# Kernel optimization log

Measured on AMD Instinct MI355X. Metric: run time of the kernel, lower is better.

## Reference

```python
import jax, jax.numpy as jnp
import numpy as np

N = 100000      # nodes
E = 1600000     # edges (avg degree 16)
IN = 128        # in_channels
H = 128         # hidden_channels
EPS = 1e-5      # BatchNorm eps


def setup_inputs() -> dict:
    key = jax.random.key(0)
    ks = jax.random.split(key, 10)
    x = jax.random.normal(ks[0], (N, IN), jnp.float32)
    edge_index = jax.random.randint(ks[1], (2, E), 0, N, dtype=jnp.int32)

    def lin(k, i, o):
        return jax.random.normal(k, (i, o), jnp.float32) * (1.0 / np.sqrt(i))

    d2 = 2 * H
    return {
        "x": x, "edge_index": edge_index,
        # SAGEConv 1: 128 -> 128
        "w1l": lin(ks[2], IN, H), "w1r": lin(ks[3], IN, H), "b1": jnp.zeros((H,), jnp.float32),
        "g1": jnp.ones((H,), jnp.float32), "be1": jnp.zeros((H,), jnp.float32),
        "m1": jnp.zeros((H,), jnp.float32), "v1": jnp.ones((H,), jnp.float32),
        # SAGEConv 2: 128 -> 256
        "w2l": lin(ks[4], H, d2), "w2r": lin(ks[5], H, d2), "b2": jnp.zeros((d2,), jnp.float32),
        "g2": jnp.ones((d2,), jnp.float32), "be2": jnp.zeros((d2,), jnp.float32),
        "m2": jnp.zeros((d2,), jnp.float32), "v2": jnp.ones((d2,), jnp.float32),
        # SAGEConv 3: 256 -> 256
        "w3l": lin(ks[6], d2, d2), "w3r": lin(ks[7], d2, d2), "b3": jnp.zeros((d2,), jnp.float32),
        "g3": jnp.ones((d2,), jnp.float32), "be3": jnp.zeros((d2,), jnp.float32),
        "m3": jnp.zeros((d2,), jnp.float32), "v3": jnp.ones((d2,), jnp.float32),
    }


def _sage_conv(x, src, dst, wl, wr, b):
    # PyG SAGEConv (mean aggr): out = mean_{j in N(i)} x_j @ W_l + x_i @ W_r + b
    agg = jax.ops.segment_sum(x[src], dst, num_segments=N)          # [N, d_in]
    deg = jax.ops.segment_sum(jnp.ones((src.shape[0],), x.dtype), dst, num_segments=N)
    mean = agg / jnp.maximum(deg, 1.0)[:, None]
    return mean @ wl + x @ wr + b


def _bn(x, g, b, m, v):
    # BatchNorm1d in eval mode (running stats); dropout is a no-op in eval
    return (x - m) * jax.lax.rsqrt(v + EPS) * g + b


def reference(x, edge_index,
              w1l, w1r, b1, g1, be1, m1, v1,
              w2l, w2r, b2, g2, be2, m2, v2,
              w3l, w3r, b3, g3, be3, m3, v3):
    src, dst = edge_index[0], edge_index[1]
    h = _bn(jax.nn.relu(_sage_conv(x, src, dst, w1l, w1r, b1)), g1, be1, m1, v1)
    h = _bn(jax.nn.relu(_sage_conv(h, src, dst, w2l, w2r, b2)), g2, be2, m2, v2)
    h = _bn(jax.nn.relu(_sage_conv(h, src, dst, w3l, w3r, b3)), g3, be3, m3, v3)
    return h  # [N, 2*H]
```

## Files before the change

kernel.cpp:

```cpp
#include <hip/hip_runtime.h>

#define NNODES 100000
#define NEDGES 1600000
#define EPSV 1e-5f

#define NB   391
#define BCAP 4608
#define EPB  4096

typedef __attribute__((ext_vector_type(8))) short bf16x8;
typedef __attribute__((ext_vector_type(4))) float f32x4;

__device__ __forceinline__ float bf2f(uint hi_shifted) {
    union { uint u; float f; } c; c.u = hi_shifted; return c.f;
}
__device__ __forceinline__ ushort f2bf(float f) {
    union { float f; uint u; } c; c.f = f;
    uint u = c.u;
    return (ushort)((u + 0x7fffu + ((u >> 16) & 1u)) >> 16);
}
__device__ __forceinline__ uint pack2(float f0, float f1) {
    return (uint)f2bf(f0) | ((uint)f2bf(f1) << 16);
}
__device__ __forceinline__ void acc8(float* a, uint4 v) {
    a[0] += bf2f(v.x << 16); a[1] += bf2f(v.x & 0xffff0000u);
    a[2] += bf2f(v.y << 16); a[3] += bf2f(v.y & 0xffff0000u);
    a[4] += bf2f(v.z << 16); a[5] += bf2f(v.z & 0xffff0000u);
    a[6] += bf2f(v.w << 16); a[7] += bf2f(v.w & 0xffff0000u);
}

__global__ __launch_bounds__(256) void part_kernel(
    const int* __restrict__ src, const int* __restrict__ dst,
    int* __restrict__ cursor, uint2* __restrict__ pairs, int E)
{
    __shared__ int lcnt[NB];
    __shared__ int lbase[NB];
    const int t = threadIdx.x;
    for (int i = t; i < NB; i += 256) lcnt[i] = 0;
    __syncthreads();

    const int base = blockIdx.x * EPB;
    const int lim  = min(base + EPB, E);

    for (int e = base + t; e < lim; e += 256)
        atomicAdd(&lcnt[((unsigned)dst[e]) >> 8], 1);
    __syncthreads();

    for (int i = t; i < NB; i += 256) {
        int c = lcnt[i];
        lbase[i] = c ? atomicAdd(&cursor[i], c) : 0;
        lcnt[i] = 0;
    }
    __syncthreads();

    for (int e = base + t; e < lim; e += 256) {
        int d = dst[e];
        int b = ((unsigned)d) >> 8;
        int p = lbase[b] + atomicAdd(&lcnt[b], 1);
        if (p < BCAP) pairs[(size_t)b * BCAP + p] = make_uint2((uint)src[e], (uint)d);
    }
}

__global__ __launch_bounds__(512) void bscan_kernel(const int* __restrict__ cursor,
                                                    int* __restrict__ colBase)
{
    __shared__ int s[512];
    int t = threadIdx.x;
    int v = (t < NB) ? min(cursor[t], BCAP) : 0;
    s[t] = v;
    __syncthreads();
    #pragma unroll
    for (int off = 1; off < 512; off <<= 1) {
        int a = (t >= off) ? s[t - off] : 0;
        __syncthreads();
        s[t] += a;
        __syncthreads();
    }
    if (t < NB) colBase[t] = s[t] - v;
}

__global__ __launch_bounds__(256) void csr_fin_kernel(
    const uint2* __restrict__ pairs, const int* __restrict__ cursor,
    const int* __restrict__ colBase, int* __restrict__ cnt,
    int* __restrict__ rptr, int* __restrict__ col, int n)
{
    __shared__ int lcnt[256];
    __shared__ int lofs[256];
    const int b = blockIdx.x;
    const int t = threadIdx.x;
    const int ecnt  = min(cursor[b], BCAP);
    const int cbase = colBase[b];
    const uint2* __restrict__ pp = pairs + (size_t)b * BCAP;

    lcnt[t] = 0;
    __syncthreads();
    for (int e = t; e < ecnt; e += 256)
        atomicAdd(&lcnt[pp[e].y & 255u], 1);
    __syncthreads();

    const int v = lcnt[t];
    lofs[t] = v;
    __syncthreads();
    #pragma unroll
    for (int off = 1; off < 256; off <<= 1) {
        int a = (t >= off) ? lofs[t - off] : 0;
        __syncthreads();
        lofs[t] += a;
        __syncthreads();
    }
    const int excl = lofs[t] - v;

    const int node = (b << 8) + t;
    if (node < n) {
        cnt[node]  = v;
        rptr[node] = cbase + excl + v;
    }
    __syncthreads();
    lcnt[t] = excl;
    __syncthreads();

    for (int e = t; e < ecnt; e += 256) {
        uint2 pr = pp[e];
        int p = cbase + atomicAdd(&lcnt[pr.y & 255u], 1);
        col[p] = (int)pr.x;
    }
}

__global__ void cvt_bf_kernel(const float* __restrict__ in, ushort* __restrict__ out, int n4) {
    int i = blockIdx.x * blockDim.x + threadIdx.x;
    if (i < n4) {
        float4 v = ((const float4*)in)[i];
        ushort4 o;
        o.x = f2bf(v.x); o.y = f2bf(v.y); o.z = f2bf(v.z); o.w = f2bf(v.w);
        ((ushort4*)out)[i] = o;
    }
}

__global__ void wT_all_kernel(
    const float* __restrict__ w1l, const float* __restrict__ w1r,
    const float* __restrict__ w2l, const float* __restrict__ w2r,
    const float* __restrict__ w3l, const float* __restrict__ w3r,
    ushort* __restrict__ t1l, ushort* __restrict__ t1r,
    ushort* __restrict__ t2l, ushort* __restrict__ t2r,
    ushort* __restrict__ t3l, ushort* __restrict__ t3r)
{
    int idx = blockIdx.x * blockDim.x + threadIdx.x;
    const float* w; ushort* wt; int K, Nout, i;
    if      (idx <  16384) { w = w1l; wt = t1l; K = 128; Nout = 128; i = idx; }
    else if (idx <  32768) { w = w1r; wt = t1r; K = 128; Nout = 128; i = idx - 16384; }
    else if (idx <  65536) { w = w2l; wt = t2l; K = 128; Nout = 256; i = idx - 32768; }
    else if (idx <  98304) { w = w2r; wt = t2r; K = 128; Nout = 256; i = idx - 65536; }
    else if (idx < 163840) { w = w3l; wt = t3l; K = 256; Nout = 256; i = idx - 98304; }
    else if (idx < 229376) { w = w3r; wt = t3r; K = 256; Nout = 256; i = idx - 163840; }
    else return;
    int k = i / Nout, n = i - k * Nout;
    wt[(size_t)n * K + k] = f2bf(w[i]);
}

template<int D>
__global__ __launch_bounds__(256) void gather_bf(
    const ushort* __restrict__ x, const int* __restrict__ rptr,
    const int* __restrict__ cnt, const int* __restrict__ col,
    ushort* __restrict__ agg, int n)
{
    constexpr int TPN = D / 8;
    constexpr int NPB = 256 / TPN;
    const int node = blockIdx.x * NPB + threadIdx.x / TPN;
    const int lane = threadIdx.x % TPN;
    if (node >= n) return;

    const int c   = cnt[node];
    const int end = rptr[node];
    const uint4* __restrict__ xp = (const uint4*)x + lane;

    float a[8] = {};
    int e = end - c;
    for (; e + 3 < end; e += 4) {
        int s0 = col[e], s1 = col[e + 1], s2 = col[e + 2], s3 = col[e + 3];
        uint4 v0 = xp[(size_t)s0 * TPN];
        uint4 v1 = xp[(size_t)s1 * TPN];
        uint4 v2 = xp[(size_t)s2 * TPN];
        uint4 v3 = xp[(size_t)s3 * TPN];
        acc8(a, v0); acc8(a, v1); acc8(a, v2); acc8(a, v3);
    }
    for (; e < end; ++e) acc8(a, xp[(size_t)col[e] * TPN]);

    const float inv = 1.0f / fmaxf((float)c, 1.0f);
    uint4 o;
    o.x = pack2(a[0] * inv, a[1] * inv);
    o.y = pack2(a[2] * inv, a[3] * inv);
    o.z = pack2(a[4] * inv, a[5] * inv);
    o.w = pack2(a[6] * inv, a[7] * inv);
    ((uint4*)agg)[(size_t)node * TPN + lane] = o;
}

template<int DIN, int DOUT, bool OUTF32>
__global__ __launch_bounds__(256) void mfma_layer(
    const ushort* __restrict__ xin, const ushort* __restrict__ agg,
    const ushort* __restrict__ wlT, const ushort* __restrict__ wrT,
    const float* __restrict__ bias, const float* __restrict__ gamma,
    const float* __restrict__ beta, const float* __restrict__ rmean,
    const float* __restrict__ rvar, void* __restrict__ outp, int M)
{
    constexpr int BM = 128, BN = 128, BK = 32;
    constexpr int LDA = BK + 8;
    __shared__ ushort As[BM * LDA];
    __shared__ ushort Bs[BN * LDA];

    const int tid  = threadIdx.x;
    const int lane = tid & 63;
    const int wid  = tid >> 6;
    const int wm   = (wid & 1) * 64;
    const int wn   = (wid >> 1) * 64;
    const int lr   = lane & 15;
    const int quad = lane >> 4;

    const int row0 = blockIdx.x * BM;
    const int col0 = blockIdx.y * BN;

    f32x4 acc[4][4] = {};

    const int s_row  = tid >> 2;
    const int s_koff = (tid & 3) * 8;

    #pragma unroll
    for (int phase = 0; phase < 2; ++phase) {
        const ushort* __restrict__ A = phase ? xin : agg;
        const ushort* __restrict__ W = phase ? wrT : wlT;

        for (int k0 = 0; k0 < DIN; k0 += BK) {
            int gr0 = row0 + s_row;       gr0 = gr0 < M ? gr0 : M - 1;
            int gr1 = row0 + s_row + 64;  gr1 = gr1 < M ? gr1 : M - 1;
            uint4 a0v = *(const uint4*)(A + (size_t)gr0 * DIN + k0 + s_koff);
            uint4 a1v = *(const uint4*)(A + (size_t)gr1 * DIN + k0 + s_koff);
            uint4 b0v = *(const uint4*)(W + (size_t)(col0 + s_row) * DIN + k0 + s_koff);
            uint4 b1v = *(const uint4*)(W + (size_t)(col0 + s_row + 64) * DIN + k0 + s_koff);

            __syncthreads();
            *(uint4*)&As[s_row * LDA + s_koff]        = a0v;
            *(uint4*)&As[(s_row + 64) * LDA + s_koff] = a1v;
            *(uint4*)&Bs[s_row * LDA + s_koff]        = b0v;
            *(uint4*)&Bs[(s_row + 64) * LDA + s_koff] = b1v;
            __syncthreads();

            bf16x8 af[4], bf[4];
            #pragma unroll
            for (int t = 0; t < 4; ++t) {
                af[t] = *(const bf16x8*)&As[(wm + t * 16 + lr) * LDA + quad * 8];
                bf[t] = *(const bf16x8*)&Bs[(wn + t * 16 + lr) * LDA + quad * 8];
            }
            #pragma unroll
            for (int mt = 0; mt < 4; ++mt)
                #pragma unroll
                for (int nt = 0; nt < 4; ++nt)
                    acc[mt][nt] = __builtin_amdgcn_mfma_f32_16x16x32_bf16(
                        af[mt], bf[nt], acc[mt][nt], 0, 0, 0);
        }
    }

    float bj[4], sj[4], mj[4], bej[4];
    #pragma unroll
    for (int nt = 0; nt < 4; ++nt) {
        int gc = col0 + wn + nt * 16 + lr;
        bj[nt]  = bias[gc];
        sj[nt]  = rsqrtf(rvar[gc] + EPSV) * gamma[gc];
        mj[nt]  = rmean[gc];
        bej[nt] = beta[gc];
    }
    #pragma unroll
    for (int mt = 0; mt < 4; ++mt) {
        #pragma unroll
        for (int r = 0; r < 4; ++r) {
            int grow = row0 + wm + mt * 16 + quad * 4 + r;
            if (grow < M) {
                #pragma unroll
                for (int nt = 0; nt < 4; ++nt) {
                    int gc = col0 + wn + nt * 16 + lr;
                    float h = acc[mt][nt][r] + bj[nt];
                    h = fmaxf(h, 0.0f);
                    h = (h - mj[nt]) * sj[nt] + bej[nt];
                    if (OUTF32) ((float*)outp)[(size_t)grow * DOUT + gc] = h;
                    else        ((ushort*)outp)[(size_t)grow * DOUT + gc] = f2bf(h);
                }
            }
        }
    }
}

extern "C" void kernel_launch(void* const* d_in, const int* in_sizes, int n_in,
                              void* d_out, int out_size, void* d_ws, size_t ws_size,
                              hipStream_t stream) {
    const int N = NNODES;
    const int E = NEDGES;

    const float* x   = (const float*)d_in[0];
    const int*   ei  = (const int*)d_in[1];
    const int*   src = ei;
    const int*   dst = ei + E;

    const float* w1l = (const float*)d_in[2];
    const float* w1r = (const float*)d_in[3];
    const float* b1  = (const float*)d_in[4];
    const float* g1  = (const float*)d_in[5];
    const float* be1 = (const float*)d_in[6];
    const float* m1  = (const float*)d_in[7];
    const float* v1  = (const float*)d_in[8];

    const float* w2l = (const float*)d_in[9];
    const float* w2r = (const float*)d_in[10];
    const float* b2  = (const float*)d_in[11];
    const float* g2  = (const float*)d_in[12];
    const float* be2 = (const float*)d_in[13];
    const float* m2  = (const float*)d_in[14];
    const float* v2  = (const float*)d_in[15];

    const float* w3l = (const float*)d_in[16];
    const float* w3r = (const float*)d_in[17];
    const float* b3  = (const float*)d_in[18];
    const float* g3  = (const float*)d_in[19];
    const float* be3 = (const float*)d_in[20];
    const float* m3  = (const float*)d_in[21];
    const float* v3  = (const float*)d_in[22];

    float* out = (float*)d_out;

    char*   wp      = (char*)d_ws;
    int*    cnt     = (int*)wp;     wp += (size_t)N * sizeof(int);
    int*    rptr    = (int*)wp;     wp += (size_t)N * sizeof(int);
    int*    cursor  = (int*)wp;     wp += 512 * sizeof(int);
    int*    colBase = (int*)wp;     wp += 512 * sizeof(int);
    int*    col     = (int*)wp;     wp += (size_t)E * sizeof(int);
    uint2*  pairs   = (uint2*)wp;   wp += (size_t)NB * BCAP * sizeof(uint2);
    ushort* xbf     = (ushort*)wp;  wp += (size_t)N * 128 * sizeof(ushort);
    ushort* h1      = (ushort*)wp;  wp += (size_t)N * 128 * sizeof(ushort);
    ushort* h2      = (ushort*)wp;  wp += (size_t)N * 256 * sizeof(ushort);
    ushort* aggb    = (ushort*)wp;  wp += (size_t)N * 256 * sizeof(ushort);
    ushort* w1lT    = (ushort*)wp;  wp += 128 * 128 * sizeof(ushort);
    ushort* w1rT    = (ushort*)wp;  wp += 128 * 128 * sizeof(ushort);
    ushort* w2lT    = (ushort*)wp;  wp += 256 * 128 * sizeof(ushort);
    ushort* w2rT    = (ushort*)wp;  wp += 256 * 128 * sizeof(ushort);
    ushort* w3lT    = (ushort*)wp;  wp += 256 * 256 * sizeof(ushort);
    ushort* w3rT    = (ushort*)wp;

    const int T = 256;

    hipMemsetAsync(cursor, 0, 512 * sizeof(int), stream);
    part_kernel<<<(E + EPB - 1) / EPB, 256, 0, stream>>>(src, dst, cursor, pairs, E);
    bscan_kernel<<<1, 512, 0, stream>>>(cursor, colBase);
    csr_fin_kernel<<<NB, 256, 0, stream>>>(pairs, cursor, colBase, cnt, rptr, col, N);

    cvt_bf_kernel<<<((N * 128 / 4) + T - 1) / T, T, 0, stream>>>(x, xbf, N * 128 / 4);
    wT_all_kernel<<<229376 / 256, 256, 0, stream>>>(w1l, w1r, w2l, w2r, w3l, w3r,
                                                    w1lT, w1rT, w2lT, w2rT, w3lT, w3rT);

    const dim3 g1g((N + 127) / 128, 1);
    const dim3 g2g((N + 127) / 128, 2);

    gather_bf<128><<<(N + 15) / 16, 256, 0, stream>>>(xbf, rptr, cnt, col, aggb, N);
    mfma_layer<128, 128, false><<<g1g, 256, 0, stream>>>(
        xbf, aggb, w1lT, w1rT, b1, g1, be1, m1, v1, h1, N);

    gather_bf<128><<<(N + 15) / 16, 256, 0, stream>>>(h1, rptr, cnt, col, aggb, N);
    mfma_layer<128, 256, false><<<g2g, 256, 0, stream>>>(
        h1, aggb, w2lT, w2rT, b2, g2, be2, m2, v2, h2, N);

    gather_bf<256><<<(N + 7) / 8, 256, 0, stream>>>(h2, rptr, cnt, col, aggb, N);
    mfma_layer<256, 256, true><<<g2g, 256, 0, stream>>>(
        h2, aggb, w3lT, w3rT, b3, g3, be3, m3, v3, out, N);
}
```

Measured before the change: 578.5 us.

## Gather neighbor features from FP8 copies instead of bf16

Each layer now also writes an FP8 (e4m3) copy of its node features, and the neighbor-mean gather reads those 8-bit rows instead of bf16. This halves the bytes moved by the random-access gather. The gather loop is also unrolled to eight edges. In exchange, every layer pays for extra byte-wise FP8 stores in the GEMM epilogue, and aggregation accuracy drops to FP8, which may break the reference tolerance. The x and h1 FP8 buffers reuse the partition scratch area, which is safe only because it is dead by then.

```diff
diff --git a/kernel.cpp b/kernel.cpp
--- a/kernel.cpp
+++ b/kernel.cpp
@@ -11,9 +11,15 @@
 typedef __attribute__((ext_vector_type(8))) short bf16x8;
 typedef __attribute__((ext_vector_type(4))) float f32x4;
 
-__device__ __forceinline__ float bf2f(uint hi_shifted) {
-    union { uint u; float f; } c; c.u = hi_shifted; return c.f;
-}
+#if defined(__has_builtin)
+#  if __has_builtin(__builtin_amdgcn_cvt_pk_f32_fp8) && __has_builtin(__builtin_amdgcn_cvt_pk_fp8_f32)
+#    define HAS_FP8_CVT 1
+#  endif
+#endif
+#ifndef HAS_FP8_CVT
+#  define HAS_FP8_CVT 0
+#endif
+
 __device__ __forceinline__ ushort f2bf(float f) {
     union { float f; uint u; } c; c.f = f;
     uint u = c.u;
@@ -22,11 +28,61 @@
 __device__ __forceinline__ uint pack2(float f0, float f1) {
     return (uint)f2bf(f0) | ((uint)f2bf(f1) << 16);
 }
-__device__ __forceinline__ void acc8(float* a, uint4 v) {
-    a[0] += bf2f(v.x << 16); a[1] += bf2f(v.x & 0xffff0000u);
-    a[2] += bf2f(v.y << 16); a[3] += bf2f(v.y & 0xffff0000u);
-    a[4] += bf2f(v.z << 16); a[5] += bf2f(v.z & 0xffff0000u);
-    a[6] += bf2f(v.w << 16); a[7] += bf2f(v.w & 0xffff0000u);
+
+#if !HAS_FP8_CVT
+__device__ __forceinline__ float fp8_dec1(uint b) {
+    uint e = (b >> 3) & 0xFu, m = b & 7u, s = b >> 7;
+    union { uint u; float f; } c;
+    c.u = e ? ((s << 31) | ((e + 120u) << 23) | (m << 20)) : (s << 31);
+    return c.f;
+}
+__device__ __forceinline__ uint fp8_enc1(float x) {
+    union { float f; uint u; } c; c.f = x;
+    uint u = c.u, s = u >> 31;
+    float ax = fabsf(x);
+    if (ax < 0.015625f) return s << 7;
+    if (ax > 448.0f)    return (s << 7) | 0x7Eu;
+    u = u + 0x7FFFFu + ((u >> 20) & 1u);
+    uint e = ((u >> 23) & 0xFFu) - 120u;
+    uint m = (u >> 20) & 7u;
+    if (e > 15u) return (s << 7) | 0x7Eu;
+    return (s << 7) | (e << 3) | m;
+}
+#endif
+
+__device__ __forceinline__ void accf8(float* a, uint2 v) {
+#if HAS_FP8_CVT
+    auto p0 = __builtin_amdgcn_cvt_pk_f32_fp8((int)v.x, false);
+    auto p1 = __builtin_amdgcn_cvt_pk_f32_fp8((int)v.x, true);
+    auto p2 = __builtin_amdgcn_cvt_pk_f32_fp8((int)v.y, false);
+    auto p3 = __builtin_amdgcn_cvt_pk_f32_fp8((int)v.y, true);
+    a[0] += p0[0]; a[1] += p0[1]; a[2] += p1[0]; a[3] += p1[1];
+    a[4] += p2[0]; a[5] += p2[1]; a[6] += p3[0]; a[7] += p3[1];
+#else
+    a[0] += fp8_dec1(v.x & 0xFFu);         a[1] += fp8_dec1((v.x >> 8) & 0xFFu);
+    a[2] += fp8_dec1((v.x >> 16) & 0xFFu); a[3] += fp8_dec1(v.x >> 24);
+    a[4] += fp8_dec1(v.y & 0xFFu);         a[5] += fp8_dec1((v.y >> 8) & 0xFFu);
+    a[6] += fp8_dec1((v.y >> 16) & 0xFFu); a[7] += fp8_dec1(v.y >> 24);
+#endif
+}
+
+__device__ __forceinline__ uint f2fp8(float f) {
+#if HAS_FP8_CVT
+    return ((uint)__builtin_amdgcn_cvt_pk_fp8_f32(f, f, 0, false)) & 0xFFu;
+#else
+    return fp8_enc1(f);
+#endif
+}
+
+__device__ __forceinline__ uint packf8_4(float f0, float f1, float f2, float f3) {
+#if HAS_FP8_CVT
+    int r = 0;
+    r = __builtin_amdgcn_cvt_pk_fp8_f32(f0, f1, r, false);
+    r = __builtin_amdgcn_cvt_pk_fp8_f32(f2, f3, r, true);
+    return (uint)r;
+#else
+    return fp8_enc1(f0) | (fp8_enc1(f1) << 8) | (fp8_enc1(f2) << 16) | (fp8_enc1(f3) << 24);
+#endif
 }
 
 __global__ __launch_bounds__(256) void part_kernel(
@@ -126,13 +182,15 @@
     }
 }
 
-__global__ void cvt_bf_kernel(const float* __restrict__ in, ushort* __restrict__ out, int n4) {
+__global__ void cvt_x_kernel(const float* __restrict__ in, ushort* __restrict__ outb,
+                             unsigned char* __restrict__ out8, int n4) {
     int i = blockIdx.x * blockDim.x + threadIdx.x;
     if (i < n4) {
         float4 v = ((const float4*)in)[i];
         ushort4 o;
         o.x = f2bf(v.x); o.y = f2bf(v.y); o.z = f2bf(v.z); o.w = f2bf(v.w);
-        ((ushort4*)out)[i] = o;
+        ((ushort4*)outb)[i] = o;
+        ((uint*)out8)[i] = packf8_4(v.x, v.y, v.z, v.w);
     }
 }
 
@@ -158,8 +216,8 @@
 }
 
 template<int D>
-__global__ __launch_bounds__(256) void gather_bf(
-    const ushort* __restrict__ x, const int* __restrict__ rptr,
+__global__ __launch_bounds__(256) void gather_f8(
+    const unsigned char* __restrict__ x, const int* __restrict__ rptr,
     const int* __restrict__ cnt, const int* __restrict__ col,
     ushort* __restrict__ agg, int n)
 {
@@ -171,19 +229,30 @@
 
     const int c   = cnt[node];
     const int end = rptr[node];
-    const uint4* __restrict__ xp = (const uint4*)x + lane;
+    const uint2* __restrict__ xp = (const uint2*)x + lane;
 
     float a[8] = {};
     int e = end - c;
-    for (; e + 3 < end; e += 4) {
-        int s0 = col[e], s1 = col[e + 1], s2 = col[e + 2], s3 = col[e + 3];
-        uint4 v0 = xp[(size_t)s0 * TPN];
-        uint4 v1 = xp[(size_t)s1 * TPN];
-        uint4 v2 = xp[(size_t)s2 * TPN];
-        uint4 v3 = xp[(size_t)s3 * TPN];
-        acc8(a, v0); acc8(a, v1); acc8(a, v2); acc8(a, v3);
-    }
-    for (; e < end; ++e) acc8(a, xp[(size_t)col[e] * TPN]);
+    for (; e + 7 < end; e += 8) {
+        int s0 = col[e],     s1 = col[e + 1], s2 = col[e + 2], s3 = col[e + 3];
+        int s4 = col[e + 4], s5 = col[e + 5], s6 = col[e + 6], s7 = col[e + 7];
+        uint2 v0 = xp[(size_t)s0 * TPN];
+        uint2 v1 = xp[(size_t)s1 * TPN];
+        uint2 v2 = xp[(size_t)s2 * TPN];
+        uint2 v3 = xp[(size_t)s3 * TPN];
+        uint2 v4 = xp[(size_t)s4 * TPN];
+        uint2 v5 = xp[(size_t)s5 * TPN];
+        uint2 v6 = xp[(size_t)s6 * TPN];
+        uint2 v7 = xp[(size_t)s7 * TPN];
+        accf8(a, v0); accf8(a, v1); accf8(a, v2); accf8(a, v3);
+        accf8(a, v4); accf8(a, v5); accf8(a, v6); accf8(a, v7);
+    }
+    for (; e + 1 < end; e += 2) {
+        uint2 v0 = xp[(size_t)col[e] * TPN];
+        uint2 v1 = xp[(size_t)col[e + 1] * TPN];
+        accf8(a, v0); accf8(a, v1);
+    }
+    if (e < end) accf8(a, xp[(size_t)col[e] * TPN]);
 
     const float inv = 1.0f / fmaxf((float)c, 1.0f);
     uint4 o;
@@ -194,13 +263,14 @@
     ((uint4*)agg)[(size_t)node * TPN + lane] = o;
 }
 
-template<int DIN, int DOUT, bool OUTF32>
+template<int DIN, int DOUT, bool OUTF32, bool WRITE8>
 __global__ __launch_bounds__(256) void mfma_layer(
     const ushort* __restrict__ xin, const ushort* __restrict__ agg,
     const ushort* __restrict__ wlT, const ushort* __restrict__ wrT,
     const float* __restrict__ bias, const float* __restrict__ gamma,
     const float* __restrict__ beta, const float* __restrict__ rmean,
-    const float* __restrict__ rvar, void* __restrict__ outp, int M)
+    const float* __restrict__ rvar, void* __restrict__ outp,
+    unsigned char* __restrict__ out8, int M)
 {
     constexpr int BM = 128, BN = 128, BK = 32;
     constexpr int LDA = BK + 8;
@@ -281,6 +351,7 @@
                     h = (h - mj[nt]) * sj[nt] + bej[nt];
                     if (OUTF32) ((float*)outp)[(size_t)grow * DOUT + gc] = h;
                     else        ((ushort*)outp)[(size_t)grow * DOUT + gc] = f2bf(h);
+                    if (WRITE8) out8[(size_t)grow * DOUT + gc] = (unsigned char)f2fp8(h);
                 }
             }
         }
@@ -335,6 +406,7 @@
     ushort* h1      = (ushort*)wp;  wp += (size_t)N * 128 * sizeof(ushort);
     ushort* h2      = (ushort*)wp;  wp += (size_t)N * 256 * sizeof(ushort);
     ushort* aggb    = (ushort*)wp;  wp += (size_t)N * 256 * sizeof(ushort);
+    unsigned char* h2f8 = (unsigned char*)wp; wp += (size_t)N * 256;
     ushort* w1lT    = (ushort*)wp;  wp += 128 * 128 * sizeof(ushort);
     ushort* w1rT    = (ushort*)wp;  wp += 128 * 128 * sizeof(ushort);
     ushort* w2lT    = (ushort*)wp;  wp += 256 * 128 * sizeof(ushort);
@@ -342,6 +414,9 @@
     ushort* w3lT    = (ushort*)wp;  wp += 256 * 256 * sizeof(ushort);
     ushort* w3rT    = (ushort*)wp;
 
+    unsigned char* xf8  = (unsigned char*)pairs;
+    unsigned char* h1f8 = (unsigned char*)pairs;
+
     const int T = 256;
 
     hipMemsetAsync(cursor, 0, 512 * sizeof(int), stream);
@@ -349,22 +424,22 @@
     bscan_kernel<<<1, 512, 0, stream>>>(cursor, colBase);
     csr_fin_kernel<<<NB, 256, 0, stream>>>(pairs, cursor, colBase, cnt, rptr, col, N);
 
-    cvt_bf_kernel<<<((N * 128 / 4) + T - 1) / T, T, 0, stream>>>(x, xbf, N * 128 / 4);
+    cvt_x_kernel<<<((N * 128 / 4) + T - 1) / T, T, 0, stream>>>(x, xbf, xf8, N * 128 / 4);
     wT_all_kernel<<<229376 / 256, 256, 0, stream>>>(w1l, w1r, w2l, w2r, w3l, w3r,
                                                     w1lT, w1rT, w2lT, w2rT, w3lT, w3rT);
 
     const dim3 g1g((N + 127) / 128, 1);
     const dim3 g2g((N + 127) / 128, 2);
 
-    gather_bf<128><<<(N + 15) / 16, 256, 0, stream>>>(xbf, rptr, cnt, col, aggb, N);
-    mfma_layer<128, 128, false><<<g1g, 256, 0, stream>>>(
-        xbf, aggb, w1lT, w1rT, b1, g1, be1, m1, v1, h1, N);
-
-    gather_bf<128><<<(N + 15) / 16, 256, 0, stream>>>(h1, rptr, cnt, col, aggb, N);
-    mfma_layer<128, 256, false><<<g2g, 256, 0, stream>>>(
-        h1, aggb, w2lT, w2rT, b2, g2, be2, m2, v2, h2, N);
-
-    gather_bf<256><<<(N + 7) / 8, 256, 0, stream>>>(h2, rptr, cnt, col, aggb, N);
-    mfma_layer<256, 256, true><<<g2g, 256, 0, stream>>>(
-        h2, aggb, w3lT, w3rT, b3, g3, be3, m3, v3, out, N);
-}
+    gather_f8<128><<<(N + 15) / 16, 256, 0, stream>>>(xf8, rptr, cnt, col, aggb, N);
+    mfma_layer<128, 128, false, true><<<g1g, 256, 0, stream>>>(
+        xbf, aggb, w1lT, w1rT, b1, g1, be1, m1, v1, h1, h1f8, N);
+
+    gather_f8<128><<<(N + 15) / 16, 256, 0, stream>>>(h1f8, rptr, cnt, col, aggb, N);
+    mfma_layer<128, 256, false, true><<<g2g, 256, 0, stream>>>(
+        h1, aggb, w2lT, w2rT, b2, g2, be2, m2, v2, h2, h2f8, N);
+
+    gather_f8<256><<<(N + 7) / 8, 256, 0, stream>>>(h2f8, rptr, cnt, col, aggb, N);
+    mfma_layer<256, 256, true, false><<<g2g, 256, 0, stream>>>(
+        h2, aggb, w3lT, w3rT, b3, g3, be3, m3, v3, out, nullptr, N);
+}
```

Result: faster. 494.5 us (-14.5%).
